# Kernel tuning notes

Hardware: AMD Instinct MI355X
Metric: run time of the kernel (lower is better)

## Reference

```python
import math
import jax, jax.numpy as jnp
import numpy as np


def conv2d(x, w, stride=1, padding=0, groups=1):
    return jax.lax.conv_general_dilated(
        x, w, (stride, stride), [(padding, padding), (padding, padding)],
        feature_group_count=groups, dimension_numbers=('NCHW', 'OIHW', 'NCHW'))


def bn_relu(x, g, b, eps=1e-5):
    # training-mode batchnorm (batch statistics, biased var) + ReLU
    m = x.mean(axis=(0, 2, 3), keepdims=True)
    v = x.var(axis=(0, 2, 3), keepdims=True)
    y = (x - m) * jax.lax.rsqrt(v + eps)
    return jax.nn.relu(y * g[None, :, None, None] + b[None, :, None, None])


def up2x(x):
    B, C, H, W = x.shape
    return jax.image.resize(x, (B, C, 2 * H, 2 * W), 'bilinear')


def pos2d(C, H, W):
    # faithful port of ReasonDecoder.pos2d -> [H*W, 1, C]
    dm = C // 2
    div = jnp.exp(jnp.arange(0.0, dm, 2.0) * (-(math.log(10000.0) / dm)))  # [dm//2]
    pos_w = jnp.arange(0.0, W)[:, None]
    pos_h = jnp.arange(0.0, H)[:, None]
    sw = jnp.sin(pos_w * div).T  # [dm//2, W]
    cw = jnp.cos(pos_w * div).T
    sh = jnp.sin(pos_h * div).T  # [dm//2, H]
    ch = jnp.cos(pos_h * div).T
    pe = jnp.zeros((C, H, W))
    pe = pe.at[0:dm:2].set(jnp.broadcast_to(sw[:, None, :], (dm // 2, H, W)))
    pe = pe.at[1:dm:2].set(jnp.broadcast_to(cw[:, None, :], (dm // 2, H, W)))
    pe = pe.at[dm::2].set(jnp.broadcast_to(sh[:, :, None], (dm // 2, H, W)))
    pe = pe.at[dm + 1::2].set(jnp.broadcast_to(ch[:, :, None], (dm // 2, H, W)))
    return pe.reshape(C, 1, H * W).transpose(2, 1, 0)


def setup_inputs() -> dict:
    key = jax.random.key(0)
    ks = jax.random.split(key, 32)
    B, C, H, W = 8, 512, 32, 32
    Cv = 256  # in_dim of Projector
    KS = 3
    s = 0.02
    inp = {
        'image_embeddings': jax.random.normal(ks[0], (B, C, H, W), jnp.float32),
        'sparse_prompt_embeddings': jax.random.normal(ks[1], (B, 2, C), jnp.float32),
        'state': jax.random.normal(ks[2], (B, C), jnp.float32),
        'multimask_output': 0,
        # stand-in transformer: single linear on (src + pos)
        'W_t': jax.random.normal(ks[3], (C, C), jnp.float32) * s,
        'iou_token': jax.random.normal(ks[4], (1, C), jnp.float32) * s,
        'mask_tokens': jax.random.normal(ks[5], (4, C), jnp.float32) * s,
        # Projector.vis
        'vis_conv1_w': jax.random.normal(ks[6], (2 * Cv, 2 * Cv, 3, 3), jnp.float32) * s,
        'vis_bn1_g': jnp.ones((2 * Cv,), jnp.float32),
        'vis_bn1_b': jnp.zeros((2 * Cv,), jnp.float32),
        'vis_conv2_w': jax.random.normal(ks[7], (Cv, 2 * Cv, 3, 3), jnp.float32) * s,
        'vis_bn2_g': jnp.ones((Cv,), jnp.float32),
        'vis_bn2_b': jnp.zeros((Cv,), jnp.float32),
        'vis_conv3_w': jax.random.normal(ks[8], (Cv, Cv, 1, 1), jnp.float32) * s,
        'vis_conv3_b': jnp.zeros((Cv,), jnp.float32),
        # Projector.txt -> Linear(512, 256*3*3 + 1)
        'txt_w': jax.random.normal(ks[9], (Cv * KS * KS + 1, C), jnp.float32) * s,
        'txt_b': jnp.zeros((Cv * KS * KS + 1,), jnp.float32),
        # 1x1 convs as linears
        'ln_ans_w': jax.random.normal(ks[10], (512, 512), jnp.float32) * s,
        'ln_ans_b': jnp.zeros((512,), jnp.float32),
        'ln_ans2_w': jax.random.normal(ks[11], (128, 512), jnp.float32) * s,
        'ln_ans2_b': jnp.zeros((128,), jnp.float32),
        # router: Linear(1024,256) -> ReLU -> Linear(256,8)
        'router_w1': jax.random.normal(ks[12], (256, 1024), jnp.float32) * s,
        'router_b1': jnp.zeros((256,), jnp.float32),
        'router_w2': jax.random.normal(ks[13], (8, 256), jnp.float32) * s,
        'router_b2': jnp.zeros((8,), jnp.float32),
        # 8 experts: Linear(128, 23) each, stacked
        'experts_w': jax.random.normal(ks[14], (8, 23, 128), jnp.float32) * s,
        'experts_b': jnp.zeros((8, 23), jnp.float32),
    }
    return inp


def reference(image_embeddings, sparse_prompt_embeddings, state, multimask_output,
              W_t, iou_token, mask_tokens,
              vis_conv1_w, vis_bn1_g, vis_bn1_b,
              vis_conv2_w, vis_bn2_g, vis_bn2_b,
              vis_conv3_w, vis_conv3_b,
              txt_w, txt_b, ln_ans_w, ln_ans_b, ln_ans2_w, ln_ans2_b,
              router_w1, router_b1, router_w2, router_b2,
              experts_w, experts_b):
    B, C, H, W = image_embeddings.shape
    pe = pos2d(C, H, W)  # [HW,1,C]

    # tokens = [iou, mask tokens, sparse prompts] (passed to transformer; hs unused)
    out_tok = jnp.concatenate([iou_token, mask_tokens], axis=0)  # [5,C]
    tokens = jnp.concatenate(
        [jnp.broadcast_to(out_tok[None], (B,) + out_tok.shape), sparse_prompt_embeddings], axis=1)
    del tokens  # hs is discarded by predict_masks

    # stand-in transformer: src_out = Linear(src_flat + pos)
    src_flat = image_embeddings.reshape(B, C, H * W).transpose(0, 2, 1) + pe[:, 0, :][None]  # [B,HW,C]
    src_flat = jnp.einsum('bnc,dc->bnd', src_flat, W_t)
    src = src_flat.transpose(0, 2, 1).reshape(B, C, H, W)

    # ---- Projector ----
    ans = src.mean(axis=(2, 3))                              # global avg pool [B,512]
    ans_vec = ans @ ln_ans_w.T + ln_ans_b                    # 1x1 conv [B,512]

    x = up2x(src)
    x = bn_relu(conv2d(x, vis_conv1_w, padding=1), vis_bn1_g, vis_bn1_b)
    x = up2x(x)
    x = bn_relu(conv2d(x, vis_conv2_w, padding=1), vis_bn2_g, vis_bn2_b)
    x = conv2d(x, vis_conv3_w) + vis_conv3_b[None, :, None, None]  # [B,256,4H,4W]
    Bx, Cx, Hx, Wx = x.shape

    qa = jnp.concatenate([state, ans_vec], axis=1)           # [B,1024]
    o = jax.nn.softmax(qa, axis=1) * qa
    half = o.shape[1] // 2
    word = o[:, :half] + o[:, half:]                         # [B,512]
    word = word @ txt_w.T + txt_b                            # [B, 256*9+1]
    dyn_w = word[:, :-1].reshape(B, Cx, 3, 3)                # per-sample conv weights
    dyn_b = word[:, -1]                                      # [B]

    xg = x.reshape(1, B * Cx, Hx, Wx)
    out = conv2d(xg, dyn_w, padding=1, groups=B) + dyn_b[None, :, None, None]  # [1,B,Hx,Wx]
    masks = out.transpose(1, 0, 2, 3)                        # [B,1,Hx,Wx]

    gates = jax.nn.softmax(
        jax.nn.relu(qa @ router_w1.T + router_b1) @ router_w2.T + router_b2, axis=1)  # [B,8]
    feat128 = ans_vec @ ln_ans2_w.T + ln_ans2_b              # [B,128]
    logits = jnp.einsum('be,eof,bf->bo', gates, experts_w, feat128) + gates @ experts_b  # [B,23]

    masks = masks[:, 1:, :, :] if multimask_output else masks[:, 0:1, :, :]
    return masks, logits, src
```

## Files before the change

### kernel.cpp

```cpp
#include <hip/hip_runtime.h>
#include <hip/hip_bf16.h>

typedef __attribute__((ext_vector_type(8))) short short8;
typedef __attribute__((ext_vector_type(4))) short shortx4;
typedef __attribute__((ext_vector_type(4))) float floatx4;

#define F2BF __float2bfloat16
#define BF2F __bfloat162float

#define WS_W4R2   0UL
#define WS_WRO2   9437184UL
#define WS_WRO1   11796480UL
#define WS_Y1     16515072UL
#define WS_Y2     50069504UL
#define WS_W4R1   50069504UL
#define WS_A      68943872UL
#define WS_WTB    77332480UL
#define WS_SRCB   77856768UL
#define WS_STATS  117178368UL
#define WS_ANS    117186560UL
#define WS_QA     117207040UL
#define WS_ANSV   117239808UL
#define WS_WORD   117256192UL
#define WS_WORD2  117272576UL
#define WS_EFFW   117346336UL
#define WS_EFFB   117420064UL
#define WS_HID    117420352UL

#define OUT_LOGITS 131072
#define OUT_SRC    131256

__device__ __forceinline__ float inp(const void* p, long i, int isbf) {
    return isbf ? BF2F(((const __hip_bfloat16*)p)[i]) : ((const float*)p)[i];
}
__device__ __forceinline__ void outw(void* p, long i, float v, int isbf) {
    if (isbf) ((__hip_bfloat16*)p)[i] = F2BF(v);
    else      ((float*)p)[i] = v;
}
__device__ __forceinline__ float bfbits2f(short s) {
    unsigned int u = ((unsigned int)(unsigned short)s) << 16;
    float f; __builtin_memcpy(&f, &u, 4); return f;
}
__device__ __forceinline__ short f2bfbits(float f) {
    __hip_bfloat16 h = F2BF(f);
    short s; __builtin_memcpy(&s, &h, 2); return s;
}

__device__ __forceinline__ int detect_bf(const void* img) {
    const unsigned short* u = (const unsigned short*)img;
    int l = threadIdx.x & 63;
    int c = 0;
#pragma unroll
    for (int k = 0; k < 8; ++k) {
        int e = (u[(l * 8 + k) * 2] >> 7) & 0xFF;
        c += (e >= 100 && e <= 150) ? 1 : 0;
    }
    for (int off = 32; off; off >>= 1) c += __shfl_xor(c, off, 64);
    return c > 307;
}

__device__ __forceinline__ float pe_val(int n, int c) {
    float pos = (c < 256) ? (float)(n & 31) : (float)(n >> 5);
    int i = ((c < 256) ? c : (c - 256)) >> 1;
    float ang = pos * expf(-0.0719557841560639f * (float)i);
    return (c & 1) ? cosf(ang) : sinf(ang);
}

__global__ void k_pre(const void* __restrict__ img, const void* __restrict__ cw1,
                      const void* __restrict__ cw2, const void* __restrict__ Wt,
                      __hip_bfloat16* __restrict__ A,
                      __hip_bfloat16* __restrict__ W4R1, __hip_bfloat16* __restrict__ W4R2,
                      __hip_bfloat16* __restrict__ WRo1, __hip_bfloat16* __restrict__ WRo2,
                      __hip_bfloat16* __restrict__ WTB) {
    int isbf = detect_bf(img);
    int bid = blockIdx.x, tid = threadIdx.x;
    __shared__ float LS[2304];
    if (bid < 4096) {
        int nt = bid & 31, ct = (bid >> 5) & 15, b = bid >> 9;
        int tx = tid & 31, ty = tid >> 5;
        int c0 = ct * 32, n0 = nt * 32;
        for (int j = 0; j < 4; ++j) {
            int c = c0 + ty + j * 8;
            LS[(ty + j * 8) * 33 + tx] = inp(img, ((long)(b * 512 + c)) * 1024 + n0 + tx, isbf);
        }
        __syncthreads();
        for (int j = 0; j < 4; ++j) {
            int n = n0 + ty + j * 8, c = c0 + tx;
            A[((long)(b * 1024 + n)) * 512 + c] = F2BF(LS[tx * 33 + ty + j * 8] + pe_val(n, c));
        }
    } else if (bid < 5632) {
        int bb = bid - 4096;
        const void* w; __hip_bfloat16 *w4, *wo; int Cout, r0;
        if (bb < 1024) { w = cw1; w4 = W4R1; wo = WRo1; Cout = 512; r0 = bb * 256; }
        else           { w = cw2; w4 = W4R2; wo = WRo2; Cout = 256; r0 = (bb - 1024) * 256; }
        int Cout4 = Cout << 2;
        int co = r0 >> 9, ci0 = r0 & 511;
        for (int e = tid; e < 2304; e += 256) LS[e] = inp(w, (long)r0 * 9 + e, isbf);
        __syncthreads();
        int ci = ci0 + tid;
        int cc = ci >> 5, cw = ci & 31;
        float w9[9];
#pragma unroll
        for (int t = 0; t < 9; ++t) w9[t] = LS[tid * 9 + t];
#pragma unroll
        for (int t = 0; t < 9; ++t)
            wo[((long)(t * 16 + cc) * Cout + co) * 32 + cw] = F2BF(w9[t]);
        const float BY[2][3][3] = {{{0.75f, 0.25f, 0.f}, {0.25f, 0.75f, 0.75f}, {0.f, 0.f, 0.25f}},
                                   {{0.25f, 0.f, 0.f},  {0.75f, 0.75f, 0.25f}, {0.f, 0.25f, 0.75f}}};
#pragma unroll
        for (int p = 0; p < 4; ++p) {
            int py = p >> 1, px = p & 1;
#pragma unroll
            for (int dy = 0; dy < 3; ++dy)
#pragma unroll
            for (int dx = 0; dx < 3; ++dx) {
                float v = 0.f;
#pragma unroll
                for (int ky = 0; ky < 3; ++ky)
#pragma unroll
                for (int kx = 0; kx < 3; ++kx)
                    v += BY[py][dy][ky] * BY[px][dx][kx] * w9[ky * 3 + kx];
                w4[((long)((dy * 3 + dx) * 16 + cc) * Cout4 + p * Cout + co) * 32 + cw] = F2BF(v);
            }
        }
    } else {
        for (int i = (bid - 5632) * 256 + tid; i < 512 * 512; i += 256 * 256)
            WTB[i] = F2BF(inp(Wt, i, isbf));
    }
}

__global__ __launch_bounds__(256) void k_gemm1(const __hip_bfloat16* __restrict__ A,
                                               const __hip_bfloat16* __restrict__ Bw,
                                               __hip_bfloat16* __restrict__ srcB,
                                               void* __restrict__ dst,
                                               float* __restrict__ ANS,
                                               const void* __restrict__ img) {
    int isbf = detect_bf(img);
    __shared__ __align__(16) __hip_bfloat16 As[128 * 32];
    __shared__ __align__(16) __hip_bfloat16 Bs[128 * 32];
    int m0 = blockIdx.x * 128, n0 = blockIdx.y * 128;
    int tid = threadIdx.x;
    int wave = tid >> 6, l = tid & 63, lm = l & 15, q = l >> 4;
    int wm = wave & 1, wn = wave >> 1;
    int m_0 = tid >> 2, qq0 = tid & 3;
    int m_1 = (tid + 256) >> 2, qq1 = qq0;
    const __hip_bfloat16* aA0 = A + ((long)(m0 + m_0)) * 512 + qq0 * 8;
    const __hip_bfloat16* aB0 = Bw + ((long)(n0 + m_0)) * 512 + qq0 * 8;
    const __hip_bfloat16* aA1 = A + ((long)(m0 + m_1)) * 512 + qq1 * 8;
    const __hip_bfloat16* aB1 = Bw + ((long)(n0 + m_1)) * 512 + qq1 * 8;
    int wA0 = m_0 * 32 + qq0 * 8, wA1 = m_1 * 32 + qq1 * 8;
    short8 rA0 = *(const short8*)(aA0), rB0 = *(const short8*)(aB0);
    short8 rA1 = *(const short8*)(aA1), rB1 = *(const short8*)(aB1);
    floatx4 zero4 = {0.f, 0.f, 0.f, 0.f};
    floatx4 acc[4][4];
    for (int i = 0; i < 4; ++i) for (int j = 0; j < 4; ++j) acc[i][j] = zero4;
    for (int k0 = 0; k0 < 512; k0 += 32) {
        __syncthreads();
        *(short8*)(As + wA0) = rA0; *(short8*)(Bs + wA0) = rB0;
        *(short8*)(As + wA1) = rA1; *(short8*)(Bs + wA1) = rB1;
        __syncthreads();
        if (k0 < 480) {
            rA0 = *(const short8*)(aA0 + k0 + 32); rB0 = *(const short8*)(aB0 + k0 + 32);
            rA1 = *(const short8*)(aA1 + k0 + 32); rB1 = *(const short8*)(aB1 + k0 + 32);
        }
        short8 af[4], bfv[4];
#pragma unroll
        for (int t = 0; t < 4; ++t) af[t] = *(short8*)(As + (wm * 64 + t * 16 + lm) * 32 + q * 8);
#pragma unroll
        for (int t = 0; t < 4; ++t) bfv[t] = *(short8*)(Bs + (wn * 64 + t * 16 + lm) * 32 + q * 8);
#pragma unroll
        for (int i = 0; i < 4; ++i)
#pragma unroll
            for (int j = 0; j < 4; ++j)
                acc[i][j] = __builtin_amdgcn_mfma_f32_16x16x32_bf16(af[i], bfv[j], acc[i][j], 0, 0, 0);
    }
    int b = m0 >> 10, hw0 = m0 & 1023;
    float cs[4] = {0.f, 0.f, 0.f, 0.f};
#pragma unroll
    for (int i = 0; i < 4; ++i)
#pragma unroll
        for (int j = 0; j < 4; ++j) {
            int mrow = wm * 64 + i * 16 + q * 4;
            int n = n0 + wn * 64 + j * 16 + lm;
            long mg = (long)(m0 + mrow);
#pragma unroll
            for (int r = 0; r < 4; ++r) {
                float v = acc[i][j][r];
                srcB[(mg + r) * 512 + n] = F2BF(v);
                cs[j] += v;
            }
            long obase = (long)OUT_SRC + ((long)(b * 512 + n)) * 1024 + hw0 + mrow;
            if (isbf) {
                shortx4 pk = { f2bfbits(acc[i][j][0]), f2bfbits(acc[i][j][1]),
                               f2bfbits(acc[i][j][2]), f2bfbits(acc[i][j][3]) };
                *(shortx4*)((__hip_bfloat16*)dst + obase) = pk;
            } else {
                floatx4 pk = { acc[i][j][0], acc[i][j][1], acc[i][j][2], acc[i][j][3] };
                *(floatx4*)((float*)dst + obase) = pk;
            }
        }
#pragma unroll
    for (int j = 0; j < 4; ++j) {
        cs[j] += __shfl_xor(cs[j], 16);
        cs[j] += __shfl_xor(cs[j], 32);
    }
    __syncthreads();
    float* CS = (float*)Bs;
    if (wm == 1 && q == 0) {
#pragma unroll
        for (int j = 0; j < 4; ++j) CS[wn * 64 + j * 16 + lm] = cs[j];
    }
    __syncthreads();
    if (wm == 0 && q == 0) {
#pragma unroll
        for (int j = 0; j < 4; ++j) {
            int n = n0 + wn * 64 + j * 16 + lm;
            atomicAdd(ANS + b * 512 + n, cs[j] + CS[wn * 64 + j * 16 + lm]);
        }
    }
}

__global__ void k_ansvec(const float* __restrict__ ANS, const void* __restrict__ lw,
                         const void* __restrict__ lb, float* __restrict__ ansv,
                         const void* __restrict__ img) {
    int isbf = detect_bf(img);
    int b = blockIdx.x, dt = blockIdx.y, tid = threadIdx.x;
    __shared__ float aL[512];
    __shared__ float R[256];
    aL[tid] = ANS[b * 512 + tid] * (1.f / 1024.f);
    aL[tid + 256] = ANS[b * 512 + tid + 256] * (1.f / 1024.f);
    __syncthreads();
    int d = dt * 64 + (tid >> 2), cl = tid & 3;
    float acc = 0.f;
    for (int k = 0; k < 128; ++k) {
        int c = cl + 4 * k;
        acc += aL[c] * inp(lw, (long)d * 512 + c, isbf);
    }
    R[tid] = acc;
    __syncthreads();
    if (cl == 0)
        ansv[b * 512 + d] = R[tid] + R[tid + 1] + R[tid + 2] + R[tid + 3] + inp(lb, d, isbf);
}

__global__ void k_word(const float* __restrict__ ansv, const void* __restrict__ state,
                       float* __restrict__ qa, float* __restrict__ word,
                       const void* __restrict__ img) {
    int isbf = detect_bf(img);
    int b = blockIdx.x, tid = threadIdx.x;
    __shared__ float L[1024];
    __shared__ float red[256];
    L[tid] = inp(state, b * 512 + tid, isbf);
    L[tid + 256] = inp(state, b * 512 + tid + 256, isbf);
    L[tid + 512] = ansv[b * 512 + tid];
    L[tid + 768] = ansv[b * 512 + tid + 256];
    __syncthreads();
    for (int j = tid; j < 1024; j += 256) qa[b * 1024 + j] = L[j];
    float m = fmaxf(fmaxf(L[tid], L[tid + 256]), fmaxf(L[tid + 512], L[tid + 768]));
    red[tid] = m; __syncthreads();
    for (int s = 128; s > 0; s >>= 1) { if (tid < s) red[tid] = fmaxf(red[tid], red[tid + s]); __syncthreads(); }
    float M = red[0]; __syncthreads();
    float z = expf(L[tid] - M) + expf(L[tid + 256] - M) + expf(L[tid + 512] - M) + expf(L[tid + 768] - M);
    red[tid] = z; __syncthreads();
    for (int s = 128; s > 0; s >>= 1) { if (tid < s) red[tid] += red[tid + s]; __syncthreads(); }
    float Z = red[0];
    for (int j = tid; j < 512; j += 256) {
        float o1 = expf(L[j] - M) / Z * L[j];
        float o2 = expf(L[j + 512] - M) / Z * L[j + 512];
        word[b * 512 + j] = o1 + o2;
    }
}

__global__ void k_txt(const float* __restrict__ word, const void* __restrict__ tw,
                      const void* __restrict__ tb, float* __restrict__ word2,
                      const void* __restrict__ img) {
    int isbf = detect_bf(img);
    int n = blockIdx.x, tid = threadIdx.x;
    __shared__ float wL[8][512];
    __shared__ float red[256 * 8];
    for (int e = tid; e < 4096; e += 256) wL[e >> 9][e & 511] = word[e];
    __syncthreads();
    float acc[8] = {0, 0, 0, 0, 0, 0, 0, 0};
    for (int c = tid; c < 512; c += 256) {
        float tv = inp(tw, (long)n * 512 + c, isbf);
        for (int b = 0; b < 8; ++b) acc[b] += wL[b][c] * tv;
    }
    for (int b = 0; b < 8; ++b) red[tid * 8 + b] = acc[b];
    __syncthreads();
    for (int s = 128; s > 0; s >>= 1) {
        if (tid < s) for (int b = 0; b < 8; ++b) red[tid * 8 + b] += red[(tid + s) * 8 + b];
        __syncthreads();
    }
    if (tid < 8) word2[tid * 2305 + n] = red[tid] + inp(tb, n, isbf);
}

__global__ void k_eff(const float* __restrict__ word2, const void* __restrict__ w3,
                      const void* __restrict__ b3, float* __restrict__ effw,
                      float* __restrict__ effb, const void* __restrict__ img) {
    int isbf = detect_bf(img);
    int bid = blockIdx.x;
    int b = bid / 9, tap = bid - b * 9;
    int tid = threadIdx.x;
    __shared__ float dw[256];
    dw[tid] = word2[b * 2305 + tid * 9 + tap];
    __syncthreads();
    float acc = 0.f;
    for (int c = 0; c < 256; ++c) acc += dw[c] * inp(w3, c * 256 + tid, isbf);
    effw[(b * 9 + tap) * 256 + tid] = acc;
    if (tid == 0) {
        float e = 0.f;
        for (int c = 0; c < 256; ++c) e += dw[c] * inp(b3, c, isbf);
        effb[b * 9 + tap] = e;
    }
}

__global__ __launch_bounds__(256, 3) void k_conv4(const __hip_bfloat16* __restrict__ in,
        const __hip_bfloat16* __restrict__ w4, __hip_bfloat16* __restrict__ out,
        int inH, int inW, int Cout, float* __restrict__ s1o, float* __restrict__ s2o,
        const float* __restrict__ bnS1, const float* __restrict__ bnS2,
        const void* __restrict__ g, const void* __restrict__ bb, float invN,
        const void* __restrict__ img) {
    int Cout4 = Cout << 2;
    int csh = (Cout == 512) ? 9 : 8;
    int tXn = inW >> 4, tYn = inH >> 3;
    int bid = blockIdx.y;
    int tX = bid % tXn; int tmp = bid / tXn; int tY = tmp % tYn; int b = tmp / tYn;
    int co0 = blockIdx.x * 128;
    __shared__ __align__(16) __hip_bfloat16 Hs[180 * 40];
    __shared__ float scT[512], shT[512];
    int tid = threadIdx.x;
    int l = tid & 63, lm = l & 15, q = l >> 4;
    int wave = tid >> 6;
    int wm = wave & 1, wn = wave >> 1;
    int dobn = (bnS1 != nullptr);
    if (dobn) {
        int isbf = detect_bf(img);
        for (int c = tid; c < 512; c += 256) {
            float m = bnS1[c] * invN, var = bnS2[c] * invN - m * m;
            float sc = inp(g, c, isbf) * rsqrtf(var + 1e-5f);
            scT[c] = sc; shT[c] = inp(bb, c, isbf) - m * sc;
        }
    }
    int R0 = (tY << 3) - 1, C0 = (tX << 4) - 1;
    long base = (long)b * inH * inW;
    int sub = tid & 3;
    const __hip_bfloat16* ga[3];
    int wo[3];
#pragma unroll
    for (int s = 0; s < 3; ++s) {
        int gi = tid + s * 256;
        int p = gi >> 2; if (p > 179) p = 179;
        int hy = p / 18, hx = p - hy * 18;
        int gr = R0 + hy; gr = gr < 0 ? 0 : (gr > inH - 1 ? inH - 1 : gr);
        int gc = C0 + hx; gc = gc < 0 ? 0 : (gc > inW - 1 ? inW - 1 : gc);
        ga[s] = in + (base + (long)gr * inW + gc) * 512 + sub * 8;
        wo[s] = p * 40 + sub * 8;
    }
    int has2 = (tid < 208);
    short8 r0 = *(const short8*)(ga[0]);
    short8 r1 = *(const short8*)(ga[1]);
    short8 r2 = {0, 0, 0, 0, 0, 0, 0, 0};
    if (has2) r2 = *(const short8*)(ga[2]);
    floatx4 zero4 = {0.f, 0.f, 0.f, 0.f};
    floatx4 acc[4][4];
    for (int i = 0; i < 4; ++i) for (int j = 0; j < 4; ++j) acc[i][j] = zero4;
    for (int ci0 = 0; ci0 < 512; ci0 += 32) {
        __syncthreads();
        if (dobn) {
            float scv[8], shv[8];
#pragma unroll
            for (int k = 0; k < 8; ++k) { int c = ci0 + sub * 8 + k; scv[k] = scT[c]; shv[k] = shT[c]; }
#pragma unroll
            for (int k = 0; k < 8; ++k) {
                float f0 = bfbits2f(r0[k]) * scv[k] + shv[k]; r0[k] = f2bfbits(f0 > 0.f ? f0 : 0.f);
                float f1 = bfbits2f(r1[k]) * scv[k] + shv[k]; r1[k] = f2bfbits(f1 > 0.f ? f1 : 0.f);
                float f2 = bfbits2f(r2[k]) * scv[k] + shv[k]; r2[k] = f2bfbits(f2 > 0.f ? f2 : 0.f);
            }
        }
        *(short8*)(Hs + wo[0]) = r0;
        *(short8*)(Hs + wo[1]) = r1;
        if (has2) *(short8*)(Hs + wo[2]) = r2;
        __syncthreads();
        if (ci0 < 480) {
            r0 = *(const short8*)(ga[0] + ci0 + 32);
            r1 = *(const short8*)(ga[1] + ci0 + 32);
            if (has2) r2 = *(const short8*)(ga[2] + ci0 + 32);
        }
        int cc = ci0 >> 5;
#pragma unroll
        for (int tap = 0; tap < 9; ++tap) {
            int dy = tap / 3, dx = tap - dy * 3;
            short8 bfv[4];
#pragma unroll
            for (int j = 0; j < 4; ++j)
                bfv[j] = *(const short8*)(w4 + ((long)(tap * 16 + cc) * Cout4 + co0 + wn * 64 + j * 16 + lm) * 32 + q * 8);
            short8 af[4];
#pragma unroll
            for (int i = 0; i < 4; ++i) {
                int py = wm * 4 + i;
                af[i] = *(const short8*)(Hs + ((py + dy) * 18 + lm + dx) * 40 + q * 8);
            }
#pragma unroll
            for (int i = 0; i < 4; ++i)
#pragma unroll
                for (int j = 0; j < 4; ++j)
                    acc[i][j] = __builtin_amdgcn_mfma_f32_16x16x32_bf16(af[i], bfv[j], acc[i][j], 0, 0, 0);
        }
    }
    int OW2 = inW << 1;
    float s1v[4] = {0.f, 0.f, 0.f, 0.f}, s2v[4] = {0.f, 0.f, 0.f, 0.f};
#pragma unroll
    for (int i = 0; i < 4; ++i)
#pragma unroll
    for (int j = 0; j < 4; ++j) {
        int co4 = co0 + wn * 64 + j * 16 + lm;
        int par = co4 >> csh;
        int co = co4 & (Cout - 1);
        int py_ = par >> 1, px_ = par & 1;
#pragma unroll
        for (int rr = 0; rr < 4; ++rr) {
            int p = wm * 64 + i * 16 + q * 4 + rr;
            int fy = ((tY << 3) + (p >> 4)) * 2 + py_;
            int fx = ((tX << 4) + (p & 15)) * 2 + px_;
            float v = acc[i][j][rr];
            out[(((long)(b * OW2 + fy)) * OW2 + fx) * Cout + co] = F2BF(v);
            s1v[j] += v; s2v[j] += v * v;
        }
    }
#pragma unroll
    for (int j = 0; j < 4; ++j) {
        s1v[j] += __shfl_xor(s1v[j], 16); s1v[j] += __shfl_xor(s1v[j], 32);
        s2v[j] += __shfl_xor(s2v[j], 16); s2v[j] += __shfl_xor(s2v[j], 32);
    }
    __syncthreads();
    float* RB = (float*)Hs;
    if (wm == 1 && q == 0) {
#pragma unroll
        for (int j = 0; j < 4; ++j) {
            int idx = wn * 64 + j * 16 + lm;
            RB[idx] = s1v[j]; RB[128 + idx] = s2v[j];
        }
    }
    __syncthreads();
    if (wm == 0 && q == 0) {
#pragma unroll
        for (int j = 0; j < 4; ++j) {
            int idx = wn * 64 + j * 16 + lm;
            int ch = (co0 + idx) & (Cout - 1);
            atomicAdd(s1o + ch, s1v[j] + RB[idx]);
            atomicAdd(s2o + ch, s2v[j] + RB[128 + idx]);
        }
    }
}

__global__ __launch_bounds__(256) void k_efix(const __hip_bfloat16* __restrict__ in,
        __hip_bfloat16* __restrict__ Y, const __hip_bfloat16* __restrict__ wRo,
        int inW, int Cout, int ebase,
        float* __restrict__ s1o, float* __restrict__ s2o) {
    int OW = inW << 1;
    int coT = Cout >> 6;
    int b = blockIdx.x / coT, cot = blockIdx.x - b * coT;
    int co0 = cot << 6;
    int e = ebase + blockIdx.y;
    __shared__ __align__(16) __hip_bfloat16 E[130 * 40];
    __shared__ __align__(16) __hip_bfloat16 Lline[64 * 32];
    int tid = threadIdx.x;
    int wave = tid >> 6, l = tid & 63, lm = l & 15, q = l >> 4;
    int mspan = OW >> 2;
    int ilim = OW >> 6;
    int mb = wave * mspan;
    floatx4 zero4 = {0.f, 0.f, 0.f, 0.f};
    floatx4 acc[2][4];
    for (int i = 0; i < 2; ++i) for (int j = 0; j < 4; ++j) acc[i][j] = zero4;
    int lineG = inW * 4;
    int eG = (OW + 2) * 4;
    int haveL = (tid < lineG);
    const __hip_bfloat16* lbase = in;
    {
        int x = tid >> 2, sb = tid & 3;
        long gidx;
        if (e < 2) { int R = (e == 0) ? 0 : inW - 1; gidx = (long)(b * inW + R) * inW + x; }
        else       { int Cc = (e == 2) ? 0 : inW - 1; gidx = (long)(b * inW + x) * inW + Cc; }
        if (x >= inW) gidx = (long)b * inW * inW;
        lbase = in + gidx * 512 + sb * 8;
    }
    short8 rl = {0, 0, 0, 0, 0, 0, 0, 0};
    if (haveL) rl = *(const short8*)(lbase);
    for (int ci0 = 0; ci0 < 512; ci0 += 32) {
        __syncthreads();
        if (haveL) *(short8*)(Lline + tid * 8) = rl;
        __syncthreads();
        if (ci0 < 480 && haveL) rl = *(const short8*)(lbase + ci0 + 32);
        for (int t = tid; t < eG; t += 256) {
            int f1 = t >> 2, sb = t & 3;
            int f = f1 - 1;
            short8 res = {0, 0, 0, 0, 0, 0, 0, 0};
            if (f < 0 || f >= OW) {
                if (e < 2) { int xx = (f < 0) ? 0 : inW - 1; res = *(const short8*)(Lline + (xx * 4 + sb) * 8); }
            } else {
                int x0; float w0;
                if (f & 1) { x0 = f >> 1; w0 = 0.75f; } else { x0 = (f >> 1) - 1; w0 = 0.25f; }
                int x1 = x0 + 1;
                if (x0 < 0) x0 = 0;
                if (x1 > inW - 1) x1 = inW - 1;
                short8 v0 = *(const short8*)(Lline + (x0 * 4 + sb) * 8);
                short8 v1 = *(const short8*)(Lline + (x1 * 4 + sb) * 8);
                float w1c = 1.f - w0;
#pragma unroll
                for (int k = 0; k < 8; ++k)
                    res[k] = f2bfbits(w0 * bfbits2f(v0[k]) + w1c * bfbits2f(v1[k]));
            }
            *(short8*)(E + f1 * 40 + sb * 8) = res;
        }
        __syncthreads();
        int cc = ci0 >> 5;
#pragma unroll
        for (int t = 0; t < 3; ++t) {
            int tap = (e == 0) ? t : (e == 1) ? (6 + t) : (e == 2) ? (t * 3) : (t * 3 + 2);
            short8 bfv[4];
#pragma unroll
            for (int j = 0; j < 4; ++j)
                bfv[j] = *(const short8*)(wRo + ((long)(tap * 16 + cc) * Cout + co0 + j * 16 + lm) * 32 + q * 8);
#pragma unroll
            for (int i = 0; i < 2; ++i) {
                if (i < ilim) {
                    short8 af = *(const short8*)(E + (mb + i * 16 + lm + t) * 40 + q * 8);
#pragma unroll
                    for (int j = 0; j < 4; ++j)
                        acc[i][j] = __builtin_amdgcn_mfma_f32_16x16x32_bf16(af, bfv[j], acc[i][j], 0, 0, 0);
                }
            }
        }
    }
    float d1s[4] = {0.f, 0.f, 0.f, 0.f}, d2s[4] = {0.f, 0.f, 0.f, 0.f};
    for (int i = 0; i < ilim; ++i)
#pragma unroll
    for (int j = 0; j < 4; ++j) {
        int co = co0 + j * 16 + lm;
#pragma unroll
        for (int r = 0; r < 4; ++r) {
            int m = mb + i * 16 + q * 4 + r;
            int fy, fx;
            if (e == 0) { fy = 0; fx = m; }
            else if (e == 1) { fy = OW - 1; fx = m; }
            else if (e == 2) { fy = m; fx = 0; }
            else { fy = m; fx = OW - 1; }
            long a = (((long)(b * OW + fy)) * OW + fx) * Cout + co;
            float vo = BF2F(Y[a]);
            float vn = vo - acc[i][j][r];
            Y[a] = F2BF(vn);
            d1s[j] += vn - vo;
            d2s[j] += vn * vn - vo * vo;
        }
    }
#pragma unroll
    for (int j = 0; j < 4; ++j) {
        d1s[j] += __shfl_xor(d1s[j], 16); d1s[j] += __shfl_xor(d1s[j], 32);
        d2s[j] += __shfl_xor(d2s[j], 16); d2s[j] += __shfl_xor(d2s[j], 32);
    }
    if (q == 0) {
#pragma unroll
        for (int j = 0; j < 4; ++j) {
            atomicAdd(s1o + co0 + j * 16 + lm, d1s[j]);
            atomicAdd(s2o + co0 + j * 16 + lm, d2s[j]);
        }
    }
}

__global__ __launch_bounds__(256) void k_masks(const __hip_bfloat16* __restrict__ x2,
                                               const float* __restrict__ effw,
                                               const float* __restrict__ effb,
                                               const float* __restrict__ word2,
                                               void* __restrict__ mout,
                                               const float* __restrict__ s1,
                                               const float* __restrict__ s2,
                                               const void* __restrict__ g,
                                               const void* __restrict__ bb, float invN,
                                               const void* __restrict__ img) {
    int isbf = detect_bf(img);
    int bid = blockIdx.x;
    int tX = bid & 15, tY = (bid >> 4) & 15, b = bid >> 8;
    __shared__ __align__(16) __hip_bfloat16 H[100 * 264];
    __shared__ __align__(16) float EW[9 * 256];
    __shared__ float EB[9];
    __shared__ float sc2T[256];
    __shared__ float sh2T[256];
    int tid = threadIdx.x;
    {
        float m = s1[tid] * invN, var = s2[tid] * invN - m * m;
        float sc = inp(g, tid, isbf) * rsqrtf(var + 1e-5f);
        sc2T[tid] = sc; sh2T[tid] = inp(bb, tid, isbf) - m * sc;
    }
    __syncthreads();
    for (int e = tid; e < 3200; e += 256) {
        int c8 = e & 31, p = e >> 5;
        int hy = p / 10, hx = p - hy * 10;
        int gy = tY * 8 + hy - 1, gx = tX * 8 + hx - 1;
        short8 res = {0, 0, 0, 0, 0, 0, 0, 0};
        if (gy >= 0 && gy < 128 && gx >= 0 && gx < 128) {
            short8 raw = *(const short8*)(x2 + (((long)(b * 128 + gy)) * 128 + gx) * 256 + c8 * 8);
#pragma unroll
            for (int k = 0; k < 8; ++k) {
                int c = c8 * 8 + k;
                float v = bfbits2f(raw[k]) * sc2T[c] + sh2T[c];
                res[k] = f2bfbits(v > 0.f ? v : 0.f);
            }
        }
        *(short8*)(H + p * 264 + c8 * 8) = res;
    }
    for (int e = tid; e < 2304; e += 256) EW[e] = effw[b * 2304 + e];
    if (tid < 9) EB[tid] = effb[b * 9 + tid];
    __syncthreads();
    int px = tid & 63, part = tid >> 6;
    int py = px >> 3, pxc = px & 7;
    int cbase = part * 64;
    float acc = 0.f;
    for (int tap = 0; tap < 9; ++tap) {
        int ky = tap / 3, kx = tap - ky * 3;
        int hp = (py + ky) * 10 + pxc + kx;
        const __hip_bfloat16* hrow = H + (long)hp * 264 + cbase;
        const float* erow = EW + tap * 256 + cbase;
#pragma unroll
        for (int c8 = 0; c8 < 8; ++c8) {
            short8 h8 = *(const short8*)(hrow + c8 * 8);
            floatx4 e0 = *(const floatx4*)(erow + c8 * 8);
            floatx4 e1 = *(const floatx4*)(erow + c8 * 8 + 4);
            acc += bfbits2f(h8[0]) * e0[0] + bfbits2f(h8[1]) * e0[1] +
                   bfbits2f(h8[2]) * e0[2] + bfbits2f(h8[3]) * e0[3] +
                   bfbits2f(h8[4]) * e1[0] + bfbits2f(h8[5]) * e1[1] +
                   bfbits2f(h8[6]) * e1[2] + bfbits2f(h8[7]) * e1[3];
        }
    }
    float (*red)[64] = (float(*)[64])sc2T;
    red[part][px] = acc;
    __syncthreads();
    if (part == 0) {
        float s = red[0][px] + red[1][px] + red[2][px] + red[3][px];
        int oy = tY * 8 + py, ox = tX * 8 + pxc;
        float bias = word2[b * 2305 + 2304];
        for (int tap = 0; tap < 9; ++tap) {
            int ky = tap / 3, kx = tap - ky * 3;
            int iy = oy + ky - 1, ix = ox + kx - 1;
            if (iy >= 0 && iy < 128 && ix >= 0 && ix < 128) bias += EB[tap];
        }
        outw(mout, b * 16384 + oy * 128 + ox, s + bias, isbf);
    }
}

__global__ void k_hid(const float* __restrict__ qa, const void* __restrict__ w1,
                      const void* __restrict__ b1, float* __restrict__ hid,
                      const void* __restrict__ img) {
    int isbf = detect_bf(img);
    int b = blockIdx.x, ht = blockIdx.y, tid = threadIdx.x;
    __shared__ float qL[1024];
    __shared__ float R[256];
    for (int j = tid; j < 1024; j += 256) qL[j] = qa[b * 1024 + j];
    __syncthreads();
    int h = ht * 64 + (tid >> 2), cl = tid & 3;
    float acc = 0.f;
    for (int k = 0; k < 256; ++k) {
        int c = cl + 4 * k;
        acc += qL[c] * inp(w1, (long)h * 1024 + c, isbf);
    }
    R[tid] = acc;
    __syncthreads();
    if (cl == 0) {
        float v = R[tid] + R[tid + 1] + R[tid + 2] + R[tid + 3] + inp(b1, h, isbf);
        hid[b * 256 + h] = v > 0.f ? v : 0.f;
    }
}

__global__ void k_logits(const float* __restrict__ hid, const float* __restrict__ ansv,
                         const void* __restrict__ w2, const void* __restrict__ b2,
                         const void* __restrict__ lw2, const void* __restrict__ lb2,
                         const void* __restrict__ ew, const void* __restrict__ ebias,
                         void* __restrict__ out, const void* __restrict__ img) {
    int isbf = detect_bf(img);
    int b = blockIdx.x, tid = threadIdx.x;
    __shared__ float hidL[256], avL[512], gates[8], feat[128], R[256];
    hidL[tid] = hid[b * 256 + tid];
    for (int j = tid; j < 512; j += 256) avL[j] = ansv[b * 512 + j];
    __syncthreads();
    if (tid < 8) {
        float gl = inp(b2, tid, isbf);
        for (int j = 0; j < 256; ++j) gl += hidL[j] * inp(w2, tid * 256 + j, isbf);
        gates[tid] = gl;
    }
    int f = tid >> 1, half = tid & 1;
    float acc = 0.f;
    for (int k = 0; k < 256; ++k) {
        int c = half + 2 * k;
        acc += avL[c] * inp(lw2, (long)f * 512 + c, isbf);
    }
    R[tid] = acc;
    __syncthreads();
    if (tid == 0) {
        float mx = gates[0];
        for (int e = 1; e < 8; ++e) mx = fmaxf(mx, gates[e]);
        float z = 0.f;
        for (int e = 0; e < 8; ++e) { gates[e] = expf(gates[e] - mx); z += gates[e]; }
        for (int e = 0; e < 8; ++e) gates[e] /= z;
    }
    if (half == 0) feat[f] = R[tid] + R[tid + 1] + inp(lb2, f, isbf);
    __syncthreads();
    if (tid < 23) {
        float a = 0.f;
        for (int e = 0; e < 8; ++e) {
            float d = inp(ebias, e * 23 + tid, isbf);
            for (int ff = 0; ff < 128; ++ff) d += inp(ew, (e * 23 + tid) * 128 + ff, isbf) * feat[ff];
            a += gates[e] * d;
        }
        outw(out, OUT_LOGITS + b * 23 + tid, a, isbf);
    }
}

extern "C" void kernel_launch(void* const* d_in, const int* in_sizes, int n_in,
                              void* d_out, int out_size, void* d_ws, size_t ws_size,
                              hipStream_t stream) {
    (void)in_sizes; (void)n_in; (void)out_size; (void)ws_size;
    const void* img   = d_in[0];
    const void* state = d_in[2];
    const void* Wt    = d_in[4];
    const void* cw1   = d_in[7];
    const void* g1    = d_in[8];
    const void* bb1   = d_in[9];
    const void* cw2   = d_in[10];
    const void* g2    = d_in[11];
    const void* bb2   = d_in[12];
    const void* w3    = d_in[13];
    const void* b3    = d_in[14];
    const void* txtw  = d_in[15];
    const void* txtb  = d_in[16];
    const void* lnw   = d_in[17];
    const void* lnb   = d_in[18];
    const void* lnw2  = d_in[19];
    const void* lnb2  = d_in[20];
    const void* rw1   = d_in[21];
    const void* rb1   = d_in[22];
    const void* rw2   = d_in[23];
    const void* rb2   = d_in[24];
    const void* ew    = d_in[25];
    const void* eb    = d_in[26];

    char* ws = (char*)d_ws;
    __hip_bfloat16* W4R2 = (__hip_bfloat16*)(ws + WS_W4R2);
    __hip_bfloat16* WRO2 = (__hip_bfloat16*)(ws + WS_WRO2);
    __hip_bfloat16* WRO1 = (__hip_bfloat16*)(ws + WS_WRO1);
    __hip_bfloat16* Y1   = (__hip_bfloat16*)(ws + WS_Y1);
    __hip_bfloat16* Y2   = (__hip_bfloat16*)(ws + WS_Y2);
    __hip_bfloat16* W4R1 = (__hip_bfloat16*)(ws + WS_W4R1);
    __hip_bfloat16* A    = (__hip_bfloat16*)(ws + WS_A);
    __hip_bfloat16* WTB  = (__hip_bfloat16*)(ws + WS_WTB);
    __hip_bfloat16* SRCB = (__hip_bfloat16*)(ws + WS_SRCB);
    float* S1A = (float*)(ws + WS_STATS);
    float* S2A = S1A + 512;
    float* S1B = S1A + 1024;
    float* S2B = S1A + 1536;
    float* ANS   = (float*)(ws + WS_ANS);
    float* QA    = (float*)(ws + WS_QA);
    float* ANSV  = (float*)(ws + WS_ANSV);
    float* WORD  = (float*)(ws + WS_WORD);
    float* WORD2 = (float*)(ws + WS_WORD2);
    float* EFFW  = (float*)(ws + WS_EFFW);
    float* EFFB  = (float*)(ws + WS_EFFB);
    float* HID   = (float*)(ws + WS_HID);

    hipMemsetAsync(ws + WS_STATS, 0, 24576, stream);

    k_pre<<<5888, 256, 0, stream>>>(img, cw1, cw2, Wt, A, W4R1, W4R2, WRO1, WRO2, WTB);
    k_gemm1<<<dim3(64, 4), 256, 0, stream>>>(A, WTB, SRCB, d_out, ANS, img);
    k_ansvec<<<dim3(8, 8), 256, 0, stream>>>(ANS, lnw, lnb, ANSV, img);
    k_word<<<8, 256, 0, stream>>>(ANSV, state, QA, WORD, img);
    k_txt<<<2305, 256, 0, stream>>>(WORD, txtw, txtb, WORD2, img);
    k_eff<<<72, 256, 0, stream>>>(WORD2, w3, b3, EFFW, EFFB, img);
    k_conv4<<<dim3(16, 64), 256, 0, stream>>>(SRCB, W4R1, Y1, 32, 32, 512, S1A, S2A,
                                              nullptr, nullptr, nullptr, nullptr, 0.f, img);
    k_efix<<<dim3(64, 2), 256, 0, stream>>>(SRCB, Y1, WRO1, 32, 512, 0, S1A, S2A);
    k_efix<<<dim3(64, 2), 256, 0, stream>>>(SRCB, Y1, WRO1, 32, 512, 2, S1A, S2A);
    k_conv4<<<dim3(8, 256), 256, 0, stream>>>(Y1, W4R2, Y2, 64, 64, 256, S1B, S2B,
                                              S1A, S2A, g1, bb1, 1.f / 32768.f, img);
    k_efix<<<dim3(32, 2), 256, 0, stream>>>(Y1, Y2, WRO2, 64, 256, 0, S1B, S2B);
    k_efix<<<dim3(32, 2), 256, 0, stream>>>(Y1, Y2, WRO2, 64, 256, 2, S1B, S2B);
    k_masks<<<2048, 256, 0, stream>>>(Y2, EFFW, EFFB, WORD2, d_out,
                                      S1B, S2B, g2, bb2, 1.f / 131072.f, img);
    k_hid<<<dim3(8, 4), 256, 0, stream>>>(QA, rw1, rb1, HID, img);
    k_logits<<<8, 256, 0, stream>>>(HID, ANSV, rw2, rb2, lnw2, lnb2, ew, eb, d_out, img);
}
```

Baseline: 1.121 ms.

## Switch conv4 to 32x32x16 MFMA tiles with register-prefetched weights

The conv4 inner loop moves from a 4x4 grid of 16x16x32 bf16 MFMAs to a 2x2 grid of 32x32x16 MFMAs per wave, with the fragment address math recomputed and the epilogue and BN statistics reduction rewritten for the 32x32 output layout. Weight fragments are now loaded one tap ahead into rotating register sets (wS0/wS1/wS2), so the global load latency overlaps the MFMAs of the current tap. The aim is fewer LDS fragment loads per FLOP and hidden weight-load latency. The cost is more register pressure under launch_bounds(256,3), which may cause spills.

```diff
diff --git a/kernel.cpp b/kernel.cpp
--- a/kernel.cpp
+++ b/kernel.cpp
@@ -4,6 +4,7 @@
 typedef __attribute__((ext_vector_type(8))) short short8;
 typedef __attribute__((ext_vector_type(4))) short shortx4;
 typedef __attribute__((ext_vector_type(4))) float floatx4;
+typedef __attribute__((ext_vector_type(16))) float floatx16;
 
 #define F2BF __float2bfloat16
 #define BF2F __bfloat162float
@@ -313,6 +314,23 @@
     }
 }
 
+__device__ __forceinline__ void epi32(const floatx16& Acc, int pxbase, int co4,
+        int csh, int Cout, int tY, int tX, int b, int OW2, int hi,
+        __hip_bfloat16* __restrict__ out, float& s1, float& s2) {
+    int par = co4 >> csh; int co = co4 & (Cout - 1);
+    int fyo = par >> 1, fxo = par & 1;
+#pragma unroll
+    for (int r = 0; r < 16; ++r) {
+        int row = (r & 3) + 8 * (r >> 2) + 4 * hi;
+        int px = pxbase + row;
+        int fy = (((tY << 3) + (px >> 4)) << 1) + fyo;
+        int fx = (((tX << 4) + (px & 15)) << 1) + fxo;
+        float v = Acc[r];
+        out[(((long)(b * OW2 + fy)) * OW2 + fx) * Cout + co] = F2BF(v);
+        s1 += v; s2 += v * v;
+    }
+}
+
 __global__ __launch_bounds__(256, 3) void k_conv4(const __hip_bfloat16* __restrict__ in,
         const __hip_bfloat16* __restrict__ w4, __hip_bfloat16* __restrict__ out,
         int inH, int inW, int Cout, float* __restrict__ s1o, float* __restrict__ s2o,
@@ -328,7 +346,7 @@
     __shared__ __align__(16) __hip_bfloat16 Hs[180 * 40];
     __shared__ float scT[512], shT[512];
     int tid = threadIdx.x;
-    int l = tid & 63, lm = l & 15, q = l >> 4;
+    int l = tid & 63, l31 = l & 31, hi = l >> 5;
     int wave = tid >> 6;
     int wm = wave & 1, wn = wave >> 1;
     int dobn = (bnS1 != nullptr);
@@ -360,10 +378,25 @@
     short8 r1 = *(const short8*)(ga[1]);
     short8 r2 = {0, 0, 0, 0, 0, 0, 0, 0};
     if (has2) r2 = *(const short8*)(ga[2]);
-    floatx4 zero4 = {0.f, 0.f, 0.f, 0.f};
-    floatx4 acc[4][4];
-    for (int i = 0; i < 4; ++i) for (int j = 0; j < 4; ++j) acc[i][j] = zero4;
+    int hb0, hb1;
+    {
+        int px0 = wm * 64 + l31;
+        int px1 = px0 + 32;
+        hb0 = ((px0 >> 4) * 18 + (px0 & 15)) * 40 + hi * 8;
+        hb1 = ((px1 >> 4) * 18 + (px1 & 15)) * 40 + hi * 8;
+    }
+    const __hip_bfloat16* wl = w4 + ((long)(co0 + wn * 64 + l31)) * 32 + hi * 8;
+    long TS = (long)Cout4 * 512;
+    long CS = (long)Cout4 * 32;
+    short8 wS0[4], wS1[4], wS2[4];
+#define LDW(S, t, c) { const __hip_bfloat16* _p = wl + (long)(t) * TS + (long)(c) * CS; \
+    S[0] = *(const short8*)(_p);            S[1] = *(const short8*)(_p + 16); \
+    S[2] = *(const short8*)(_p + 1024);     S[3] = *(const short8*)(_p + 1024 + 16); }
+    floatx16 zero16 = {0,0,0,0,0,0,0,0,0,0,0,0,0,0,0,0};
+    floatx16 a00 = zero16, a01 = zero16, a10 = zero16, a11 = zero16;
+    LDW(wS0, 0, 0);
     for (int ci0 = 0; ci0 < 512; ci0 += 32) {
+        int cc = ci0 >> 5;
         __syncthreads();
         if (dobn) {
             float scv[8], shv[8];
@@ -385,70 +418,81 @@
             r1 = *(const short8*)(ga[1] + ci0 + 32);
             if (has2) r2 = *(const short8*)(ga[2] + ci0 + 32);
         }
-        int cc = ci0 >> 5;
 #pragma unroll
         for (int tap = 0; tap < 9; ++tap) {
+            {
+                int nt = tap + 1, ncc = cc;
+                if (nt == 9) { nt = 0; ncc = cc + 1; }
+                if (ncc < 16) {
+                    if (((tap + 1) % 3) == 0)      { LDW(wS0, nt, ncc); }
+                    else if (((tap + 1) % 3) == 1) { LDW(wS1, nt, ncc); }
+                    else                            { LDW(wS2, nt, ncc); }
+                }
+            }
             int dy = tap / 3, dx = tap - dy * 3;
-            short8 bfv[4];
-#pragma unroll
-            for (int j = 0; j < 4; ++j)
-                bfv[j] = *(const short8*)(w4 + ((long)(tap * 16 + cc) * Cout4 + co0 + wn * 64 + j * 16 + lm) * 32 + q * 8);
-            short8 af[4];
-#pragma unroll
-            for (int i = 0; i < 4; ++i) {
-                int py = wm * 4 + i;
-                af[i] = *(const short8*)(Hs + ((py + dy) * 18 + lm + dx) * 40 + q * 8);
+            int ho = (dy * 18 + dx) * 40;
+            short8 af00 = *(const short8*)(Hs + hb0 + ho);
+            short8 af01 = *(const short8*)(Hs + hb0 + ho + 16);
+            short8 af10 = *(const short8*)(Hs + hb1 + ho);
+            short8 af11 = *(const short8*)(Hs + hb1 + ho + 16);
+            if ((tap % 3) == 0) {
+                a00 = __builtin_amdgcn_mfma_f32_32x32x16_bf16(af00, wS0[0], a00, 0, 0, 0);
+                a00 = __builtin_amdgcn_mfma_f32_32x32x16_bf16(af01, wS0[1], a00, 0, 0, 0);
+                a01 = __builtin_amdgcn_mfma_f32_32x32x16_bf16(af00, wS0[2], a01, 0, 0, 0);
+                a01 = __builtin_amdgcn_mfma_f32_32x32x16_bf16(af01, wS0[3], a01, 0, 0, 0);
+                a10 = __builtin_amdgcn_mfma_f32_32x32x16_bf16(af10, wS0[0], a10, 0, 0, 0);
+                a10 = __builtin_amdgcn_mfma_f32_32x32x16_bf16(af11, wS0[1], a10, 0, 0, 0);
+                a11 = __builtin_amdgcn_mfma_f32_32x32x16_bf16(af10, wS0[2], a11, 0, 0, 0);
+                a11 = __builtin_amdgcn_mfma_f32_32x32x16_bf16(af11, wS0[3], a11, 0, 0, 0);
+            } else if ((tap % 3) == 1) {
+                a00 = __builtin_amdgcn_mfma_f32_32x32x16_bf16(af00, wS1[0], a00, 0, 0, 0);
+                a00 = __builtin_amdgcn_mfma_f32_32x32x16_bf16(af01, wS1[1], a00, 0, 0, 0);
+                a01 = __builtin_amdgcn_mfma_f32_32x32x16_bf16(af00, wS1[2], a01, 0, 0, 0);
+                a01 = __builtin_amdgcn_mfma_f32_32x32x16_bf16(af01, wS1[3], a01, 0, 0, 0);
+                a10 = __builtin_amdgcn_mfma_f32_32x32x16_bf16(af10, wS1[0], a10, 0, 0, 0);
+                a10 = __builtin_amdgcn_mfma_f32_32x32x16_bf16(af11, wS1[1], a10, 0, 0, 0);
+                a11 = __builtin_amdgcn_mfma_f32_32x32x16_bf16(af10, wS1[2], a11, 0, 0, 0);
+                a11 = __builtin_amdgcn_mfma_f32_32x32x16_bf16(af11, wS1[3], a11, 0, 0, 0);
+            } else {
+                a00 = __builtin_amdgcn_mfma_f32_32x32x16_bf16(af00, wS2[0], a00, 0, 0, 0);
+                a00 = __builtin_amdgcn_mfma_f32_32x32x16_bf16(af01, wS2[1], a00, 0, 0, 0);
+                a01 = __builtin_amdgcn_mfma_f32_32x32x16_bf16(af00, wS2[2], a01, 0, 0, 0);
+                a01 = __builtin_amdgcn_mfma_f32_32x32x16_bf16(af01, wS2[3], a01, 0, 0, 0);
+                a10 = __builtin_amdgcn_mfma_f32_32x32x16_bf16(af10, wS2[0], a10, 0, 0, 0);
+                a10 = __builtin_amdgcn_mfma_f32_32x32x16_bf16(af11, wS2[1], a10, 0, 0, 0);
+                a11 = __builtin_amdgcn_mfma_f32_32x32x16_bf16(af10, wS2[2], a11, 0, 0, 0);
+                a11 = __builtin_amdgcn_mfma_f32_32x32x16_bf16(af11, wS2[3], a11, 0, 0, 0);
             }
-#pragma unroll
-            for (int i = 0; i < 4; ++i)
-#pragma unroll
-                for (int j = 0; j < 4; ++j)
-                    acc[i][j] = __builtin_amdgcn_mfma_f32_16x16x32_bf16(af[i], bfv[j], acc[i][j], 0, 0, 0);
-        }
-    }
+        }
+    }
+#undef LDW
     int OW2 = inW << 1;
-    float s1v[4] = {0.f, 0.f, 0.f, 0.f}, s2v[4] = {0.f, 0.f, 0.f, 0.f};
-#pragma unroll
-    for (int i = 0; i < 4; ++i)
-#pragma unroll
-    for (int j = 0; j < 4; ++j) {
-        int co4 = co0 + wn * 64 + j * 16 + lm;
-        int par = co4 >> csh;
-        int co = co4 & (Cout - 1);
-        int py_ = par >> 1, px_ = par & 1;
-#pragma unroll
-        for (int rr = 0; rr < 4; ++rr) {
-            int p = wm * 64 + i * 16 + q * 4 + rr;
-            int fy = ((tY << 3) + (p >> 4)) * 2 + py_;
-            int fx = ((tX << 4) + (p & 15)) * 2 + px_;
-            float v = acc[i][j][rr];
-            out[(((long)(b * OW2 + fy)) * OW2 + fx) * Cout + co] = F2BF(v);
-            s1v[j] += v; s2v[j] += v * v;
-        }
-    }
-#pragma unroll
-    for (int j = 0; j < 4; ++j) {
-        s1v[j] += __shfl_xor(s1v[j], 16); s1v[j] += __shfl_xor(s1v[j], 32);
-        s2v[j] += __shfl_xor(s2v[j], 16); s2v[j] += __shfl_xor(s2v[j], 32);
-    }
+    float s1v0 = 0.f, s2v0 = 0.f, s1v1 = 0.f, s2v1 = 0.f;
+    {
+        int pxb0 = wm * 64, pxb1 = wm * 64 + 32;
+        int co4a = co0 + wn * 64 + l31;
+        int co4b = co4a + 32;
+        epi32(a00, pxb0, co4a, csh, Cout, tY, tX, b, OW2, hi, out, s1v0, s2v0);
+        epi32(a10, pxb1, co4a, csh, Cout, tY, tX, b, OW2, hi, out, s1v0, s2v0);
+        epi32(a01, pxb0, co4b, csh, Cout, tY, tX, b, OW2, hi, out, s1v1, s2v1);
+        epi32(a11, pxb1, co4b, csh, Cout, tY, tX, b, OW2, hi, out, s1v1, s2v1);
+    }
+    s1v0 += __shfl_xor(s1v0, 32); s2v0 += __shfl_xor(s2v0, 32);
+    s1v1 += __shfl_xor(s1v1, 32); s2v1 += __shfl_xor(s2v1, 32);
     __syncthreads();
     float* RB = (float*)Hs;
-    if (wm == 1 && q == 0) {
-#pragma unroll
-        for (int j = 0; j < 4; ++j) {
-            int idx = wn * 64 + j * 16 + lm;
-            RB[idx] = s1v[j]; RB[128 + idx] = s2v[j];
-        }
-    }
-    __syncthreads();
-    if (wm == 0 && q == 0) {
-#pragma unroll
-        for (int j = 0; j < 4; ++j) {
-            int idx = wn * 64 + j * 16 + lm;
-            int ch = (co0 + idx) & (Cout - 1);
-            atomicAdd(s1o + ch, s1v[j] + RB[idx]);
-            atomicAdd(s2o + ch, s2v[j] + RB[128 + idx]);
-        }
+    if (wm == 1 && hi == 0) {
+        int i0 = wn * 64 + l31, i1 = i0 + 32;
+        RB[i0] = s1v0; RB[128 + i0] = s2v0;
+        RB[i1] = s1v1; RB[128 + i1] = s2v1;
+    }
+    __syncthreads();
+    if (wm == 0 && hi == 0) {
+        int i0 = wn * 64 + l31, i1 = i0 + 32;
+        atomicAdd(s1o + ((co0 + i0) & (Cout - 1)), s1v0 + RB[i0]);
+        atomicAdd(s2o + ((co0 + i0) & (Cout - 1)), s2v0 + RB[128 + i0]);
+        atomicAdd(s1o + ((co0 + i1) & (Cout - 1)), s1v1 + RB[i1]);
+        atomicAdd(s2o + ((co0 + i1) & (Cout - 1)), s2v1 + RB[128 + i1]);
     }
 }
 
```

New measurement: 1.094 ms. 1.03x faster.
